# Optimization experiments

Hardware: AMD Instinct MI355X
Metric: run time of the kernel (lower is better)

The kernel has to match this reference:

```python
import jax, jax.numpy as jnp
import numpy as np

BS, H, W = 32, 768, 768


def setup_inputs() -> dict:
    key = jax.random.key(0)
    k1, k2 = jax.random.split(key)
    im = jax.random.normal(k1, (BS, 3, H, W), dtype=jnp.float32)
    flat_col = jax.random.normal(k2, (BS, 37), dtype=jnp.float32) * 0.1
    return {"im": im, "flat_col": flat_col}


def reference(im, flat_col):
    bs, c, h, w = im.shape  # c == 3
    colwarp = flat_col[:, :9].reshape(bs, 3, 3)          # per-sample 3x3 color matrix
    colshift = flat_col[:, 9:12][:, :, None, None]        # per-sample per-channel shift
    spatial = flat_col[:, 12:].reshape(bs, 1, 5, 5)       # per-sample 5x5 kernel, shared across channels

    x = im + colshift
    x = jnp.einsum('bdhw,bdc->bchw', x, colwarp)

    # Batched per-sample depthwise conv expressed as ONE grouped conv:
    # fold (batch, channel) into the feature dim and use feature_group_count = bs*3.
    k = jnp.broadcast_to(spatial, (bs, 3, 5, 5)).reshape(bs * 3, 1, 5, 5)
    xi = x.reshape(1, bs * 3, h, w)
    out = jax.lax.conv_general_dilated(
        xi, k,
        window_strides=(1, 1),
        padding=((2, 2), (2, 2)),
        dimension_numbers=('NCHW', 'OIHW', 'NCHW'),
        feature_group_count=bs * 3,
    )
    return out.reshape(bs, 3, h, w)
```

## Files before the change

### kernel.cpp

```cpp
#include <hip/hip_runtime.h>

#define NB 32
#define CH 3
#define HH 768
#define WW 768

#define TW 64
#define TH 16
#define SW 72
#define SWP 76
#define SH (TH + 4)
#define CSTRIDE (SH * SWP)
#define TPB 8
#define NTC (WW / TW)
#define NTG (HH / (TH * TPB))
#define NWG (NB * NTC * NTG)
#define UNITS (SH * (SW / 4))

typedef float v4f __attribute__((ext_vector_type(4)));

__device__ inline int pswz(int s) { return s ^ (((s >> 5) & 1) << 1); }

__global__ __launch_bounds__(256) void colwarp_conv_kernel(
    const float* __restrict__ im,
    const float* __restrict__ flat,
    float* __restrict__ out)
{
    const int d   = blockIdx.x;
    const int wid = (d & 7) * (NWG / 8) + (d >> 3);
    const int tc  = wid % NTC;
    const int t2  = wid / NTC;
    const int tg  = t2 % NTG;
    const int b   = t2 / NTG;
    const int tw0 = tc * TW;
    const int thbase = tg * (TPB * TH);

    __shared__ float xs[CH][SH][SWP];

    const int tid = threadIdx.x;

    const float* f = flat + b * 37;
    float Wm[3][3];
#pragma unroll
    for (int i = 0; i < 3; ++i)
#pragma unroll
        for (int j = 0; j < 3; ++j) Wm[i][j] = f[i * 3 + j];
    float sh3[3];
#pragma unroll
    for (int i = 0; i < 3; ++i) sh3[i] = f[9 + i];
    float K[5][5];
#pragma unroll
    for (int i = 0; i < 5; ++i)
#pragma unroll
        for (int j = 0; j < 5; ++j) K[i][j] = f[12 + i * 5 + j];
    float bias[3];
#pragma unroll
    for (int c = 0; c < 3; ++c)
        bias[c] = sh3[0]*Wm[0][c] + sh3[1]*Wm[1][c] + sh3[2]*Wm[2][c];

    const size_t plane = (size_t)HH * WW;
    const float* im0 = im + (size_t)b * CH * plane;

    int ur[2], uldso[2], ugw[2];
    bool uon[2], uswap[2];
#pragma unroll
    for (int ui = 0; ui < 2; ++ui) {
        const int u  = tid + 256 * ui;
        const int rr = u / (SW / 4);
        const int c4 = u - rr * (SW / 4);
        ur[ui]    = rr;
        uldso[ui] = rr * SWP + c4 * 4;
        ugw[ui]   = tw0 - 4 + c4 * 4;
        uon[ui]   = (u < UNITS);
        uswap[ui] = ((c4 >> 3) & 1) != 0;
    }

    float4 vld[2][CH];
    bool vok[2];

#define STAGE_LOAD(TH0)                                                        \
    _Pragma("unroll")                                                          \
    for (int ui = 0; ui < 2; ++ui) {                                           \
        const int gh = (TH0) + ur[ui] - 2;                                     \
        const bool ok = uon[ui] && ((unsigned)gh < (unsigned)HH)               \
                                && ((unsigned)ugw[ui] < (unsigned)WW);         \
        vok[ui] = ok;                                                          \
        if (ok) {                                                              \
            const size_t off = (size_t)gh * WW + ugw[ui];                      \
            vld[ui][0] = *(const float4*)(im0 + off);                          \
            vld[ui][1] = *(const float4*)(im0 + plane + off);                  \
            vld[ui][2] = *(const float4*)(im0 + 2 * plane + off);              \
        }                                                                      \
    }

#define STAGE_WRITE(BUFP)                                                      \
    _Pragma("unroll")                                                          \
    for (int ui = 0; ui < 2; ++ui) {                                           \
        if (uon[ui]) {                                                         \
            float4 m0 = make_float4(0.f, 0.f, 0.f, 0.f), m1 = m0, m2 = m0;     \
            if (vok[ui]) {                                                     \
                const float4 a0 = vld[ui][0], a1 = vld[ui][1], a2 = vld[ui][2];\
                m0.x = a0.x*Wm[0][0] + a1.x*Wm[1][0] + a2.x*Wm[2][0] + bias[0];\
                m0.y = a0.y*Wm[0][0] + a1.y*Wm[1][0] + a2.y*Wm[2][0] + bias[0];\
                m0.z = a0.z*Wm[0][0] + a1.z*Wm[1][0] + a2.z*Wm[2][0] + bias[0];\
                m0.w = a0.w*Wm[0][0] + a1.w*Wm[1][0] + a2.w*Wm[2][0] + bias[0];\
                m1.x = a0.x*Wm[0][1] + a1.x*Wm[1][1] + a2.x*Wm[2][1] + bias[1];\
                m1.y = a0.y*Wm[0][1] + a1.y*Wm[1][1] + a2.y*Wm[2][1] + bias[1];\
                m1.z = a0.z*Wm[0][1] + a1.z*Wm[1][1] + a2.z*Wm[2][1] + bias[1];\
                m1.w = a0.w*Wm[0][1] + a1.w*Wm[1][1] + a2.w*Wm[2][1] + bias[1];\
                m2.x = a0.x*Wm[0][2] + a1.x*Wm[1][2] + a2.x*Wm[2][2] + bias[2];\
                m2.y = a0.y*Wm[0][2] + a1.y*Wm[1][2] + a2.y*Wm[2][2] + bias[2];\
                m2.z = a0.z*Wm[0][2] + a1.z*Wm[1][2] + a2.z*Wm[2][2] + bias[2];\
                m2.w = a0.w*Wm[0][2] + a1.w*Wm[1][2] + a2.w*Wm[2][2] + bias[2];\
            }                                                                  \
            const bool sw = uswap[ui];                                         \
            const float4 w0 = sw ? make_float4(m0.z,m0.w,m0.x,m0.y) : m0;      \
            const float4 w1 = sw ? make_float4(m1.z,m1.w,m1.x,m1.y) : m1;      \
            const float4 w2 = sw ? make_float4(m2.z,m2.w,m2.x,m2.y) : m2;      \
            *(float4*)((BUFP) + 0 * CSTRIDE + uldso[ui]) = w0;                 \
            *(float4*)((BUFP) + 1 * CSTRIDE + uldso[ui]) = w1;                 \
            *(float4*)((BUFP) + 2 * CSTRIDE + uldso[ui]) = w2;                 \
        }                                                                      \
    }

    const int tx = tid & 15;
    const int ty = tid >> 4;
    const int r0 = ty;

    const int offA = pswz(4 * tx + 2);
    const int offB = pswz(4 * tx + 4);
    const int offC = pswz(4 * tx + 6);
    const int offD = pswz(4 * tx + 8);

#define CONV_STORE(BUFP, TH0)                                                  \
    {                                                                          \
        float acc[CH][4];                                                      \
        _Pragma("unroll")                                                      \
        for (int c = 0; c < CH; ++c)                                           \
            _Pragma("unroll")                                                  \
            for (int o = 0; o < 4; ++o) acc[c][o] = 0.f;                       \
        _Pragma("unroll")                                                      \
        for (int rr = 0; rr < 5; ++rr) {                                       \
            _Pragma("unroll")                                                  \
            for (int c = 0; c < CH; ++c) {                                     \
                const float* rowb = (BUFP) + c * CSTRIDE + (r0 + rr) * SWP;    \
                const float2 p0 = *(const float2*)(rowb + offA);               \
                const float2 p1 = *(const float2*)(rowb + offB);               \
                const float2 p2 = *(const float2*)(rowb + offC);               \
                const float2 p3 = *(const float2*)(rowb + offD);               \
                const float w8[8] = {p0.x, p0.y, p1.x, p1.y,                   \
                                     p2.x, p2.y, p3.x, p3.y};                  \
                _Pragma("unroll")                                              \
                for (int j = 0; j < 5; ++j) {                                  \
                    _Pragma("unroll")                                          \
                    for (int o = 0; o < 4; ++o)                                \
                        acc[c][o] += w8[o + j] * K[rr][j];                     \
                }                                                              \
            }                                                                  \
        }                                                                      \
        _Pragma("unroll")                                                      \
        for (int c = 0; c < CH; ++c) {                                         \
            float* ob = out + ((size_t)b * CH + c) * plane;                    \
            v4f vv = {acc[c][0], acc[c][1], acc[c][2], acc[c][3]};             \
            __builtin_nontemporal_store(vv,                                    \
                (v4f*)&ob[(size_t)((TH0) + r0) * WW + tw0 + tx * 4]);          \
        }                                                                      \
    }

    STAGE_LOAD(thbase);
    STAGE_WRITE(&xs[0][0][0]);
    __syncthreads();

#pragma unroll 1
    for (int t = 0; t < TPB; ++t) {
        const int th0 = thbase + t * TH;
        if (t + 1 < TPB) { STAGE_LOAD(th0 + TH); }
        CONV_STORE(&xs[0][0][0], th0);
        __syncthreads();
        if (t + 1 < TPB) {
            STAGE_WRITE(&xs[0][0][0]);
            __syncthreads();
        }
    }
}

extern "C" void kernel_launch(void* const* d_in, const int* in_sizes, int n_in,
                              void* d_out, int out_size, void* d_ws, size_t ws_size,
                              hipStream_t stream) {
    const float* im   = (const float*)d_in[0];
    const float* flat = (const float*)d_in[1];
    float* out        = (float*)d_out;

    colwarp_conv_kernel<<<dim3(NWG), dim3(256), 0, stream>>>(im, flat, out);
}
```

Measured before the change: 80.99 us.

## Flatten tile schedule so fixed 2048 workgroups each process 9 consecutive tiles

The work split changes from 3072 workgroups with 8 row-tiles each to exactly 2048 workgroups with 9 tiles each. Tiles are laid out along flattened column strips, and a workgroup reloads its per-sample parameters and restages its halo whenever it crosses into a new strip. The aim is better load balance across CUs, presumably 2048 = 8 per CU on 256 CUs, in a single wave. In exchange, workgroups that cross a strip boundary pay an extra unpipelined load and sync, and the kernel now needs 18432 tiles to divide exactly by 2048.

```diff
diff --git a/kernel.cpp b/kernel.cpp
--- a/kernel.cpp
+++ b/kernel.cpp
@@ -11,10 +11,11 @@
 #define SWP 76
 #define SH (TH + 4)
 #define CSTRIDE (SH * SWP)
-#define TPB 8
 #define NTC (WW / TW)
-#define NTG (HH / (TH * TPB))
-#define NWG (NB * NTC * NTG)
+#define NCOL (NB * NTC)
+#define TPC (HH / TH)
+#define NWG 2048
+#define TPB 9
 #define UNITS (SH * (SW / 4))
 
 typedef float v4f __attribute__((ext_vector_type(4)));
@@ -28,40 +29,20 @@
 {
     const int d   = blockIdx.x;
     const int wid = (d & 7) * (NWG / 8) + (d >> 3);
-    const int tc  = wid % NTC;
-    const int t2  = wid / NTC;
-    const int tg  = t2 % NTG;
-    const int b   = t2 / NTG;
-    const int tw0 = tc * TW;
-    const int thbase = tg * (TPB * TH);
 
     __shared__ float xs[CH][SH][SWP];
 
     const int tid = threadIdx.x;
 
-    const float* f = flat + b * 37;
-    float Wm[3][3];
-#pragma unroll
-    for (int i = 0; i < 3; ++i)
-#pragma unroll
-        for (int j = 0; j < 3; ++j) Wm[i][j] = f[i * 3 + j];
-    float sh3[3];
-#pragma unroll
-    for (int i = 0; i < 3; ++i) sh3[i] = f[9 + i];
-    float K[5][5];
-#pragma unroll
-    for (int i = 0; i < 5; ++i)
-#pragma unroll
-        for (int j = 0; j < 5; ++j) K[i][j] = f[12 + i * 5 + j];
-    float bias[3];
-#pragma unroll
-    for (int c = 0; c < 3; ++c)
-        bias[c] = sh3[0]*Wm[0][c] + sh3[1]*Wm[1][c] + sh3[2]*Wm[2][c];
+    int curcol = -1;
+    int tw0 = 0;
+    float Wm[3][3], sh3[3], K[5][5], bias[3];
+    const float *cb0 = im, *cb1 = im, *cb2 = im;
+    float *ob0 = out, *ob1 = out, *ob2 = out;
 
     const size_t plane = (size_t)HH * WW;
-    const float* im0 = im + (size_t)b * CH * plane;
-
-    int ur[2], uldso[2], ugw[2];
+
+    int ur[2], uldso[2], uc4[2];
     bool uon[2], uswap[2];
 #pragma unroll
     for (int ui = 0; ui < 2; ++ui) {
@@ -70,10 +51,11 @@
         const int c4 = u - rr * (SW / 4);
         ur[ui]    = rr;
         uldso[ui] = rr * SWP + c4 * 4;
-        ugw[ui]   = tw0 - 4 + c4 * 4;
+        uc4[ui]   = c4;
         uon[ui]   = (u < UNITS);
         uswap[ui] = ((c4 >> 3) & 1) != 0;
     }
+    int ugw[2] = {0, 0};
 
     float4 vld[2][CH];
     bool vok[2];
@@ -87,13 +69,13 @@
         vok[ui] = ok;                                                          \
         if (ok) {                                                              \
             const size_t off = (size_t)gh * WW + ugw[ui];                      \
-            vld[ui][0] = *(const float4*)(im0 + off);                          \
-            vld[ui][1] = *(const float4*)(im0 + plane + off);                  \
-            vld[ui][2] = *(const float4*)(im0 + 2 * plane + off);              \
-        }                                                                      \
-    }
-
-#define STAGE_WRITE(BUFP)                                                      \
+            vld[ui][0] = *(const float4*)(cb0 + off);                          \
+            vld[ui][1] = *(const float4*)(cb1 + off);                          \
+            vld[ui][2] = *(const float4*)(cb2 + off);                          \
+        }                                                                      \
+    }
+
+#define STAGE_WRITE()                                                          \
     _Pragma("unroll")                                                          \
     for (int ui = 0; ui < 2; ++ui) {                                           \
         if (uon[ui]) {                                                         \
@@ -117,9 +99,9 @@
             const float4 w0 = sw ? make_float4(m0.z,m0.w,m0.x,m0.y) : m0;      \
             const float4 w1 = sw ? make_float4(m1.z,m1.w,m1.x,m1.y) : m1;      \
             const float4 w2 = sw ? make_float4(m2.z,m2.w,m2.x,m2.y) : m2;      \
-            *(float4*)((BUFP) + 0 * CSTRIDE + uldso[ui]) = w0;                 \
-            *(float4*)((BUFP) + 1 * CSTRIDE + uldso[ui]) = w1;                 \
-            *(float4*)((BUFP) + 2 * CSTRIDE + uldso[ui]) = w2;                 \
+            *(float4*)(&xs[0][0][0] + 0 * CSTRIDE + uldso[ui]) = w0;           \
+            *(float4*)(&xs[0][0][0] + 1 * CSTRIDE + uldso[ui]) = w1;           \
+            *(float4*)(&xs[0][0][0] + 2 * CSTRIDE + uldso[ui]) = w2;           \
         }                                                                      \
     }
 
@@ -132,7 +114,7 @@
     const int offC = pswz(4 * tx + 6);
     const int offD = pswz(4 * tx + 8);
 
-#define CONV_STORE(BUFP, TH0)                                                  \
+#define CONV_STORE(TH0)                                                        \
     {                                                                          \
         float acc[CH][4];                                                      \
         _Pragma("unroll")                                                      \
@@ -143,7 +125,8 @@
         for (int rr = 0; rr < 5; ++rr) {                                       \
             _Pragma("unroll")                                                  \
             for (int c = 0; c < CH; ++c) {                                     \
-                const float* rowb = (BUFP) + c * CSTRIDE + (r0 + rr) * SWP;    \
+                const float* rowb = &xs[0][0][0] + c * CSTRIDE                 \
+                                    + (r0 + rr) * SWP;                         \
                 const float2 p0 = *(const float2*)(rowb + offA);               \
                 const float2 p1 = *(const float2*)(rowb + offB);               \
                 const float2 p2 = *(const float2*)(rowb + offC);               \
@@ -158,27 +141,60 @@
                 }                                                              \
             }                                                                  \
         }                                                                      \
-        _Pragma("unroll")                                                      \
-        for (int c = 0; c < CH; ++c) {                                         \
-            float* ob = out + ((size_t)b * CH + c) * plane;                    \
-            v4f vv = {acc[c][0], acc[c][1], acc[c][2], acc[c][3]};             \
-            __builtin_nontemporal_store(vv,                                    \
-                (v4f*)&ob[(size_t)((TH0) + r0) * WW + tw0 + tx * 4]);          \
-        }                                                                      \
-    }
-
-    STAGE_LOAD(thbase);
-    STAGE_WRITE(&xs[0][0][0]);
-    __syncthreads();
+        {                                                                      \
+            const size_t obase = (size_t)((TH0) + r0) * WW + tw0 + tx * 4;     \
+            v4f v0 = {acc[0][0], acc[0][1], acc[0][2], acc[0][3]};             \
+            v4f v1 = {acc[1][0], acc[1][1], acc[1][2], acc[1][3]};             \
+            v4f v2 = {acc[2][0], acc[2][1], acc[2][2], acc[2][3]};             \
+            __builtin_nontemporal_store(v0, (v4f*)&ob0[obase]);                \
+            __builtin_nontemporal_store(v1, (v4f*)&ob1[obase]);                \
+            __builtin_nontemporal_store(v2, (v4f*)&ob2[obase]);                \
+        }                                                                      \
+    }
 
 #pragma unroll 1
-    for (int t = 0; t < TPB; ++t) {
-        const int th0 = thbase + t * TH;
-        if (t + 1 < TPB) { STAGE_LOAD(th0 + TH); }
-        CONV_STORE(&xs[0][0][0], th0);
+    for (int ti = 0; ti < TPB; ++ti) {
+        const int w    = wid * TPB + ti;
+        const int col  = w / TPC;
+        const int trow = w - col * TPC;
+        const int th0  = trow * TH;
+
+        if (col != curcol) {
+            curcol = col;
+            const int b  = col / NTC;
+            const int tc = col - b * NTC;
+            tw0 = tc * TW;
+            const float* f = flat + b * 37;
+#pragma unroll
+            for (int i = 0; i < 3; ++i)
+#pragma unroll
+                for (int j = 0; j < 3; ++j) Wm[i][j] = f[i * 3 + j];
+#pragma unroll
+            for (int i = 0; i < 3; ++i) sh3[i] = f[9 + i];
+#pragma unroll
+            for (int i = 0; i < 5; ++i)
+#pragma unroll
+                for (int j = 0; j < 5; ++j) K[i][j] = f[12 + i * 5 + j];
+#pragma unroll
+            for (int c = 0; c < 3; ++c)
+                bias[c] = sh3[0]*Wm[0][c] + sh3[1]*Wm[1][c] + sh3[2]*Wm[2][c];
+            const float* cbase = im + (size_t)b * CH * plane;
+            cb0 = cbase; cb1 = cbase + plane; cb2 = cbase + 2 * plane;
+            float* obase = out + (size_t)b * CH * plane;
+            ob0 = obase; ob1 = obase + plane; ob2 = obase + 2 * plane;
+#pragma unroll
+            for (int ui = 0; ui < 2; ++ui) ugw[ui] = tw0 - 4 + uc4[ui] * 4;
+            STAGE_LOAD(th0);
+            STAGE_WRITE();
+            __syncthreads();
+        }
+
+        const bool more = (ti + 1 < TPB) && (trow != TPC - 1);
+        if (more) { STAGE_LOAD(th0 + TH); }
+        CONV_STORE(th0);
         __syncthreads();
-        if (t + 1 < TPB) {
-            STAGE_WRITE(&xs[0][0][0]);
+        if (more) {
+            STAGE_WRITE();
             __syncthreads();
         }
     }
```

Measured after the change: 106.7 us. +31.7%, slower.
